# Kernel tuning notes

Measured on AMD Instinct MI355X. Metric: run time of the kernel, lower is better.

Reference implementation:

```python
import jax, jax.numpy as jnp
import numpy as np

B, C_IN, H, W = 4, 256, 64, 64
LATENT = 256


def setup_inputs() -> dict:
    key = jax.random.key(0)
    ks = jax.random.split(key, 12)
    s_in = 1.0 / np.sqrt(C_IN)
    s_lat = 1.0 / np.sqrt(LATENT)
    return {
        "x": jax.random.normal(ks[0], (B, C_IN, H, W), dtype=jnp.float32),
        # 1x1 conv weights stored as [out, in]
        "wq": jax.random.normal(ks[1], (LATENT, C_IN), dtype=jnp.float32) * s_in,
        "bq": jnp.zeros((LATENT,), dtype=jnp.float32),
        "wk": jax.random.normal(ks[2], (LATENT, C_IN), dtype=jnp.float32) * s_in,
        "bk": jnp.zeros((LATENT,), dtype=jnp.float32),
        "wv": jax.random.normal(ks[3], (LATENT, C_IN), dtype=jnp.float32) * s_in,
        "bv": jnp.zeros((LATENT,), dtype=jnp.float32),
        "w_out": jax.random.normal(ks[4], (C_IN, LATENT), dtype=jnp.float32) * s_lat,
        "b_out": jnp.zeros((C_IN,), dtype=jnp.float32),
        # positional-embedding MLP (torch nn.Linear: y = x @ W.T + b)
        "mlp_w1": jax.random.normal(ks[5], (LATENT, LATENT), dtype=jnp.float32) * s_lat,
        "mlp_b1": jnp.zeros((LATENT,), dtype=jnp.float32),
        "mlp_w2": jax.random.normal(ks[6], (LATENT, LATENT), dtype=jnp.float32) * s_lat,
        "mlp_b2": jnp.zeros((LATENT,), dtype=jnp.float32),
    }


def _sinusoidal_table(timesteps, dim):
    # embed[t, d] = sin(arg) if d even else cos(arg), arg = t / 10000**(2d/dim)
    t = jnp.arange(timesteps, dtype=jnp.float32)[:, None]
    p = jnp.arange(dim, dtype=jnp.float32)[None, :]
    w = t / jnp.power(jnp.float32(10000.0), 2.0 * p / dim)
    even = (jnp.arange(dim) % 2 == 0)[None, :]
    return jnp.where(even, jnp.sin(w), jnp.cos(w))  # [T, dim]


def _conv1x1(x, w, b):
    # x: [B, Cin, H, W], w: [Cout, Cin]
    return jnp.einsum('bchw,oc->bohw', x, w) + b[None, :, None, None]


def reference(x, wq, bq, wk, bk, wv, bv, w_out, b_out, mlp_w1, mlp_b1, mlp_w2, mlp_b2):
    batch, _, h, w_ = x.shape
    L = wq.shape[0]
    hw = h * w_

    q = _conv1x1(x, wq, bq)
    k = _conv1x1(x, wk, bk)
    v = _conv1x1(x, wv, bv)

    pe = _sinusoidal_table(hw, L)                     # [HW, L]
    pe = jax.nn.silu(pe @ mlp_w1.T + mlp_b1) @ mlp_w2.T + mlp_b2
    pe = pe.reshape(1, L, h, w_)                      # faithful to torch reshape

    q = (q + pe).reshape(batch, L, hw)
    k = (k + pe).reshape(batch, L, hw)
    v = (v + pe).reshape(batch, L, hw)

    # attention[b, i, j] = sum_c q[b, c, i] * k[b, c, j] / sqrt(L)
    att = jnp.einsum('bci,bcj->bij', q, k) / jnp.sqrt(jnp.float32(L))
    att = jax.nn.softmax(att, axis=1)                 # SAGAN-style: softmax over queries
    res = jnp.einsum('bci,bij->bcj', v, att)          # bmm(v, attention)
    res = res.reshape(batch, L, h, w_)
    return _conv1x1(res, w_out, b_out)
```

## Files before the change

kernel.cpp:

```cpp
#include <hip/hip_runtime.h>
#include <cstdint>


typedef short s8v __attribute__((ext_vector_type(8)));
typedef float f32x4 __attribute__((ext_vector_type(4)));

#define DEVI static __device__ __forceinline__

DEVI unsigned short f2bf(float f) {
  union { float f; uint32_t u; } x; x.f = f;
  uint32_t u = x.u;
  return (unsigned short)((u + 0x7fffu + ((u >> 16) & 1u)) >> 16);
}

DEVI void gl_lds16(const void* g, void* l) {
  __builtin_amdgcn_global_load_lds(
      (const __attribute__((address_space(1))) void*)g,
      (__attribute__((address_space(3))) void*)l,
      16, 0, 0);
}

DEVI void stage(const unsigned short* src, int ld, unsigned short* lds, int t) {
  gl_lds16(src + (long)(t >> 2) * ld + (t & 3) * 8, lds + (t >> 6) * 512);
}

template <int OBF, int BIAS, int PEM, int SILU>
__global__ __launch_bounds__(256) void gemm_nt(
    const unsigned short* __restrict__ A, const unsigned short* __restrict__ B,
    void* __restrict__ Cp, int K, int N, int ld, long sA, long sB, long sC,
    const float* __restrict__ bias, const float* __restrict__ pe, float scale) {
  const int bz = blockIdx.z;
  const unsigned short* Ab = A + (long)bz * sA;
  const unsigned short* Bb = B + (long)bz * sB;
  const int m0 = blockIdx.x * 128, n0 = blockIdx.y * 128;
  __shared__ __align__(16) unsigned short As[4096], Bs[4096];
  const int t = threadIdx.x;
  const int wave = t >> 6, lane = t & 63;
  const int wr = wave >> 1, wc = wave & 1;

  f32x4 acc[4][4];
#pragma unroll
  for (int i = 0; i < 4; i++)
#pragma unroll
    for (int j = 0; j < 4; j++) acc[i][j] = f32x4{0.f, 0.f, 0.f, 0.f};

  const int rl = lane & 15, kp = (lane >> 4) * 8;

  for (int k0 = 0; k0 < K; k0 += 32) {
    stage(Ab + (long)m0 * ld + k0, ld, As, t);
    stage(Ab + (long)(m0 + 64) * ld + k0, ld, As + 2048, t);
    stage(Bb + (long)n0 * ld + k0, ld, Bs, t);
    stage(Bb + (long)(n0 + 64) * ld + k0, ld, Bs + 2048, t);
    __syncthreads();

    s8v af[4], bfr[4];
#pragma unroll
    for (int i = 0; i < 4; i++)
      af[i] = *(const s8v*)(As + (wr * 64 + i * 16 + rl) * 32 + kp);
#pragma unroll
    for (int j = 0; j < 4; j++)
      bfr[j] = *(const s8v*)(Bs + (wc * 64 + j * 16 + rl) * 32 + kp);
#pragma unroll
    for (int i = 0; i < 4; i++)
#pragma unroll
      for (int j = 0; j < 4; j++)
        acc[i][j] = __builtin_amdgcn_mfma_f32_16x16x32_bf16(af[i], bfr[j],
                                                            acc[i][j], 0, 0, 0);
    __syncthreads();
  }

  const long cb = (long)bz * sC;
#pragma unroll
  for (int i = 0; i < 4; i++) {
    const int r0 = m0 + wr * 64 + i * 16 + (lane >> 4) * 4;
#pragma unroll
    for (int j = 0; j < 4; j++) {
      const int col = n0 + wc * 64 + j * 16 + (lane & 15);
#pragma unroll
      for (int r = 0; r < 4; r++) {
        const int row = r0 + r;
        float val = acc[i][j][r] * scale;
        if (BIAS == 1) val += bias[row];
        if (BIAS == 2) val += bias[col];
        if (PEM == 1) val += pe[(long)row * 4096 + col];
        if (PEM == 2) val += pe[(long)col * 4096 + row];
        if (SILU) val = val / (1.0f + __expf(-val));
        const long ci = cb + (long)row * N + col;
        if (OBF)
          ((unsigned short*)Cp)[ci] = f2bf(val);
        else
          ((float*)Cp)[ci] = val;
      }
    }
  }
}

__global__ __launch_bounds__(512, 2) void flash_attn(
    const unsigned short* __restrict__ qTp, const unsigned short* __restrict__ kTp,
    const unsigned short* __restrict__ vBp, float* __restrict__ oPart,
    float* __restrict__ lPart) {
  const int bid = blockIdx.x;
  const int xcd = bid & 7;
  const int b = xcd >> 1, ihalf = xcd & 1;
  const int j0 = (bid >> 3) * 128;
  const long S = 1048576;
  const long ibase = (long)ihalf * 2048;
  const unsigned short* q = qTp + (long)b * S;
  const unsigned short* k = kTp + (long)b * S;
  const unsigned short* v = vBp + (long)b * S;
  const int ob = b * 2 + ihalf;

  __shared__ __align__(16) unsigned char ldsb[151552];

  const int t = threadIdx.x;
  const int wave = t >> 6, lane = t & 63;
  const int jq = wave & 3, ch = wave >> 2;
  const int rl = lane & 15, g = lane >> 4;
  const int kp = g * 8;
  const int ksw = ((g ^ ((rl >> 1) & 3)) << 3);
  const int th = t >> 8, tt = t & 255;
  unsigned short* pL = (unsigned short*)(ldsb + 131072);
  unsigned short* pLw = pL + wave * 1280;

  const unsigned short* krow = k + (long)(j0 + jq * 32 + rl) * 256 + kp;
  s8v kreg[2][8];
#pragma unroll
  for (int jf = 0; jf < 2; jf++)
#pragma unroll
    for (int s = 0; s < 8; s++)
      kreg[jf][s] = *(const s8v*)(krow + jf * 16 * 256 + s * 32);

  f32x4 oacc[2][16];
#pragma unroll
  for (int jf = 0; jf < 2; jf++)
#pragma unroll
    for (int cf = 0; cf < 16; cf++) oacc[jf][cf] = f32x4{0.f, 0.f, 0.f, 0.f};
  float plsum[2][4] = {{0.f, 0.f, 0.f, 0.f}, {0.f, 0.f, 0.f, 0.f}};

  const int tr = tt >> 2, tc = tt & 3;
  const int sc = (tc ^ ((tr >> 1) & 3)) * 8;
  const unsigned short* qsrc[4];
  const unsigned short* vsrc[4];
  const int dsto = (tt >> 6) * 512;
#pragma unroll
  for (int ss = 0; ss < 4; ss++) {
    const int s_ = ss * 2 + th;
    qsrc[ss] = q + ibase * 256 + s_ * 32 + (long)tr * 256 + sc;
    vsrc[ss] = v + (long)((s_ >> 1) * 64) * 4096 + ibase + (s_ & 1) * 32 +
               (long)tr * 4096 + sc;
  }

#define STAGE_QV(bufsel)                                                     \
  {                                                                          \
    unsigned short* qD = (unsigned short*)(ldsb + ((bufsel) << 15));         \
    unsigned short* vD = (unsigned short*)(ldsb + 65536 + ((bufsel) << 15)); \
    _Pragma("unroll") for (int ss = 0; ss < 4; ss++) {                       \
      const int s_ = ss * 2 + th;                                            \
      gl_lds16(qsrc[ss], qD + s_ * 2048 + dsto);                             \
      gl_lds16(vsrc[ss], vD + s_ * 2048 + dsto);                             \
      qsrc[ss] += 16384;                     \
      vsrc[ss] += 64;                        \
    }                                                                        \
  }

  STAGE_QV(0)

  for (int n = 0; n < 32; ++n) {
    const int cur = n & 1;
    __syncthreads();
    if (n + 1 < 32) STAGE_QV(cur ^ 1)

    const unsigned short* qLb = (const unsigned short*)(ldsb + (cur << 15));
    const unsigned short* vLb =
        (const unsigned short*)(ldsb + 65536 + (cur << 15));

    f32x4 sa[2][2];
#pragma unroll
    for (int jf = 0; jf < 2; jf++)
#pragma unroll
      for (int f = 0; f < 2; f++) sa[jf][f] = f32x4{0.f, 0.f, 0.f, 0.f};
    const unsigned short* qbase = qLb + (ch * 32 + rl) * 32 + ksw;
#pragma unroll
    for (int s = 0; s < 8; s++) {
#pragma unroll
      for (int f = 0; f < 2; f++) {
        s8v bf = *(const s8v*)(qbase + s * 2048 + f * 512);
        sa[0][f] = __builtin_amdgcn_mfma_f32_16x16x32_bf16(kreg[0][s], bf,
                                                           sa[0][f], 0, 0, 0);
        sa[1][f] = __builtin_amdgcn_mfma_f32_16x16x32_bf16(kreg[1][s], bf,
                                                           sa[1][f], 0, 0, 0);
      }
    }

#pragma unroll
    for (int jf = 0; jf < 2; jf++)
#pragma unroll
      for (int f = 0; f < 2; f++)
#pragma unroll
        for (int r = 0; r < 4; r++) {
          const float p = __expf(sa[jf][f][r] * 0.0625f);
          plsum[jf][r] += p;
          pLw[jf * 640 + (g * 4 + r) * 40 + f * 16 + rl] = f2bf(p);
        }

    s8v pa0 = *(const s8v*)(pLw + rl * 40 + kp);
    s8v pa1 = *(const s8v*)(pLw + 640 + rl * 40 + kp);
    const unsigned short* vbase = vLb + ch * 2048 + rl * 32 + ksw;
#pragma unroll
    for (int cf = 0; cf < 16; cf++) {
      s8v vb = *(const s8v*)(vbase + (cf >> 2) * 4096 + (cf & 3) * 512);
      oacc[0][cf] = __builtin_amdgcn_mfma_f32_16x16x32_bf16(pa0, vb,
                                                            oacc[0][cf], 0, 0, 0);
      oacc[1][cf] = __builtin_amdgcn_mfma_f32_16x16x32_bf16(pa1, vb,
                                                            oacc[1][cf], 0, 0, 0);
    }
  }

#pragma unroll
  for (int jf = 0; jf < 2; jf++)
#pragma unroll
    for (int r = 0; r < 4; r++) {
      plsum[jf][r] += __shfl_xor(plsum[jf][r], 1);
      plsum[jf][r] += __shfl_xor(plsum[jf][r], 2);
      plsum[jf][r] += __shfl_xor(plsum[jf][r], 4);
      plsum[jf][r] += __shfl_xor(plsum[jf][r], 8);
    }

  __syncthreads();
  float* ex = (float*)ldsb;
  float* exl = (float*)(ldsb + 131072);
  if (ch == 1) {
    float* exw = ex + jq * 8192;
#pragma unroll
    for (int jf = 0; jf < 2; jf++)
#pragma unroll
      for (int cf = 0; cf < 16; cf++)
#pragma unroll
        for (int r = 0; r < 4; r++)
          exw[(jf * 16 + g * 4 + r) * 256 + cf * 16 + rl] = oacc[jf][cf][r];
    if (rl == 0) {
#pragma unroll
      for (int jf = 0; jf < 2; jf++)
#pragma unroll
        for (int r = 0; r < 4; r++)
          exl[jq * 32 + jf * 16 + g * 4 + r] = plsum[jf][r];
    }
  }
  __syncthreads();
  if (ch == 0) {
    float* exw = ex + jq * 8192;
    float* op = oPart + (long)ob * 1048576;
#pragma unroll
    for (int jf = 0; jf < 2; jf++) {
      if (rl == 0) {
#pragma unroll
        for (int r = 0; r < 4; r++) {
          const int jl = jq * 32 + jf * 16 + g * 4 + r;
          lPart[(long)ob * 4096 + j0 + jl] = plsum[jf][r] + exl[jl];
        }
      }
#pragma unroll
      for (int cf = 0; cf < 16; cf++)
#pragma unroll
        for (int r = 0; r < 4; r++) {
          const int jl2 = jf * 16 + g * 4 + r;
          op[(long)(j0 + jq * 32 + jl2) * 256 + cf * 16 + rl] =
              oacc[jf][cf][r] + exw[jl2 * 256 + cf * 16 + rl];
        }
    }
  }
#undef STAGE_QV
}

__global__ __launch_bounds__(256) void combine_o(
    const float* __restrict__ oPart, const float* __restrict__ lPart,
    unsigned short* __restrict__ rT) {
  const long idx = (long)blockIdx.x * 256 + threadIdx.x;
  const int c4 = idx & 63;
  const int j = (idx >> 6) & 4095;
  const int b = idx >> 18;
  const long p0 = ((long)(b * 2) * 1048576 + (long)j * 256) / 4 + c4;
  const float4 a = ((const float4*)oPart)[p0];
  const float4 d = ((const float4*)oPart)[p0 + 262144];
  const float l = lPart[(long)(b * 2) * 4096 + j] +
                  lPart[(long)(b * 2 + 1) * 4096 + j];
  const float inv = 1.0f / l;
  ushort4 o;
  o.x = f2bf((a.x + d.x) * inv);
  o.y = f2bf((a.y + d.y) * inv);
  o.z = f2bf((a.z + d.z) * inv);
  o.w = f2bf((a.w + d.w) * inv);
  ((ushort4*)rT)[(long)b * 262144 + (long)j * 64 + c4] = o;
}

__global__ __launch_bounds__(256) void convert6(
    const float* __restrict__ a0, const float* __restrict__ a1,
    const float* __restrict__ a2, const float* __restrict__ a3,
    const float* __restrict__ a4, const float* __restrict__ a5,
    unsigned short* __restrict__ dst) {
  int idx = blockIdx.x * 256 + threadIdx.x;
  int m = idx >> 16, r = idx & 65535;
  const float* s;
  switch (m) {
    case 0: s = a0; break;
    case 1: s = a1; break;
    case 2: s = a2; break;
    case 3: s = a3; break;
    case 4: s = a4; break;
    default: s = a5; break;
  }
  dst[idx] = f2bf(s[r]);
}

__global__ __launch_bounds__(256) void embed_k(unsigned short* __restrict__ e) {
  int idx = blockIdx.x * 256 + threadIdx.x;
  int t = idx >> 8, d = idx & 255;
  float freq = powf(10000.0f, -(float)d * (1.0f / 128.0f));
  float w = (float)t * freq;
  float r = (d & 1) ? cosf(w) : sinf(w);
  e[idx] = f2bf(r);
}

__global__ void transpose_x(const float* __restrict__ x,
                            unsigned short* __restrict__ xt) {
  __shared__ float tile[32][33];
  const int b = blockIdx.z;
  const int s0 = blockIdx.x * 32, c0 = blockIdx.y * 32;
  const int tx = threadIdx.x, ty = threadIdx.y;
  const float* xb = x + (long)b * 256 * 4096;
#pragma unroll
  for (int r = 0; r < 32; r += 8)
    tile[ty + r][tx] = xb[(long)(c0 + ty + r) * 4096 + s0 + tx];
  __syncthreads();
  unsigned short* xtb = xt + (long)b * 4096 * 256;
#pragma unroll
  for (int r = 0; r < 32; r += 8)
    xtb[(long)(s0 + ty + r) * 256 + c0 + tx] = f2bf(tile[tx][ty + r]);
}

extern "C" void kernel_launch(void* const* d_in, const int* in_sizes, int n_in,
                              void* d_out, int out_size, void* d_ws,
                              size_t ws_size, hipStream_t stream) {
  const float* x  = (const float*)d_in[0];
  const float* wq = (const float*)d_in[1];
  const float* bq = (const float*)d_in[2];
  const float* wk = (const float*)d_in[3];
  const float* bk = (const float*)d_in[4];
  const float* wv = (const float*)d_in[5];
  const float* bv = (const float*)d_in[6];
  const float* wo = (const float*)d_in[7];
  const float* bo = (const float*)d_in[8];
  const float* w1 = (const float*)d_in[9];
  const float* b1 = (const float*)d_in[10];
  const float* w2 = (const float*)d_in[11];
  const float* b2 = (const float*)d_in[12];
  float* out = (float*)d_out;

  char* ws = (char*)d_ws;
  unsigned short* wqb = (unsigned short*)(ws + 0);
  unsigned short* wkb = (unsigned short*)(ws + 131072);
  unsigned short* wvb = (unsigned short*)(ws + 262144);
  unsigned short* wob = (unsigned short*)(ws + 393216);
  unsigned short* w1b = (unsigned short*)(ws + 524288);
  unsigned short* w2b = (unsigned short*)(ws + 655360);
  unsigned short* emb = (unsigned short*)(ws + 786432);
  unsigned short* h1b = (unsigned short*)(ws + 2883584);
  float*          peF = (float*)(ws + 4980736);
  unsigned short* XT  = (unsigned short*)(ws + 9175040);
  unsigned short* qT  = (unsigned short*)(ws + 17563648);
  unsigned short* kT  = (unsigned short*)(ws + 25952256);
  unsigned short* vB  = (unsigned short*)(ws + 34340864);
  unsigned short* rT  = (unsigned short*)(ws + 42729472);
  float*          oP  = (float*)(ws + 51118080);
  float*          lP  = (float*)(ws + 84672512);
  (void)ws_size; (void)in_sizes; (void)n_in; (void)out_size;

  const dim3 B256(256);
  const long S = 1048576;

  convert6<<<1536, B256, 0, stream>>>(wq, wk, wv, wo, w1, w2, wqb);
  embed_k<<<4096, B256, 0, stream>>>(emb);
  gemm_nt<1, 2, 0, 1><<<dim3(32, 2, 1), B256, 0, stream>>>(
      emb, w1b, h1b, 256, 256, 256, 0, 0, 0, b1, nullptr, 1.0f);
  gemm_nt<0, 2, 0, 0><<<dim3(32, 2, 1), B256, 0, stream>>>(
      h1b, w2b, peF, 256, 256, 256, 0, 0, 0, b2, nullptr, 1.0f);
  transpose_x<<<dim3(128, 8, 4), dim3(32, 8), 0, stream>>>(x, XT);
  gemm_nt<1, 2, 2, 0><<<dim3(32, 2, 4), B256, 0, stream>>>(
      XT, wqb, qT, 256, 256, 256, S, 0, S, bq, peF, 1.0f);
  gemm_nt<1, 2, 2, 0><<<dim3(32, 2, 4), B256, 0, stream>>>(
      XT, wkb, kT, 256, 256, 256, S, 0, S, bk, peF, 1.0f);
  gemm_nt<1, 1, 1, 0><<<dim3(2, 32, 4), B256, 0, stream>>>(
      wvb, XT, vB, 256, 4096, 256, 0, S, S, bv, peF, 1.0f);

  flash_attn<<<256, dim3(512), 0, stream>>>(qT, kT, vB, oP, lP);
  combine_o<<<4096, B256, 0, stream>>>(oP, lP, rT);

  gemm_nt<0, 1, 0, 0><<<dim3(2, 32, 4), B256, 0, stream>>>(
      wob, rT, out, 256, 4096, 256, 0, S, S, bo, nullptr, 1.0f);
}
```

Before: 171.4 us.

## Software-pipeline attention loop so PV of previous tile overlaps QK of current

Q and V staging are split so that V for a tile is loaded one iteration later than Q. Each iteration now computes QK MFMAs for tile n, then the PV MFMAs for tile n-1 using probabilities written to LDS in the previous iteration. A final PV step after the loop handles the last tile. This reorders the loop so the exp and LDS write of P no longer sit directly between the two MFMA chains, with the aim of hiding that dependency latency. The exponential is also rewritten as exp2f with the log2(e) factor folded into the scale. One risk: the Q prefetch is no longer guarded on the last iteration, so it reads past the current range and writes into an LDS buffer that is never used.

```diff
diff --git a/kernel.cpp b/kernel.cpp
--- a/kernel.cpp
+++ b/kernel.cpp
@@ -150,36 +150,47 @@
                (long)tr * 4096 + sc;
   }
 
-#define STAGE_QV(bufsel)                                                     \
+#define STAGE_Q(bufsel)                                                      \
   {                                                                          \
     unsigned short* qD = (unsigned short*)(ldsb + ((bufsel) << 15));         \
+    _Pragma("unroll") for (int ss = 0; ss < 4; ss++) {                       \
+      const int s_ = ss * 2 + th;                                            \
+      gl_lds16(qsrc[ss], qD + s_ * 2048 + dsto);                             \
+      qsrc[ss] += 16384;                     \
+    }                                                                        \
+  }
+#define STAGE_V(bufsel)                                                      \
+  {                                                                          \
     unsigned short* vD = (unsigned short*)(ldsb + 65536 + ((bufsel) << 15)); \
     _Pragma("unroll") for (int ss = 0; ss < 4; ss++) {                       \
       const int s_ = ss * 2 + th;                                            \
-      gl_lds16(qsrc[ss], qD + s_ * 2048 + dsto);                             \
       gl_lds16(vsrc[ss], vD + s_ * 2048 + dsto);                             \
-      qsrc[ss] += 16384;                     \
       vsrc[ss] += 64;                        \
     }                                                                        \
   }
 
-  STAGE_QV(0)
+  STAGE_Q(0)
 
   for (int n = 0; n < 32; ++n) {
     const int cur = n & 1;
     __syncthreads();
-    if (n + 1 < 32) STAGE_QV(cur ^ 1)
-
-    const unsigned short* qLb = (const unsigned short*)(ldsb + (cur << 15));
-    const unsigned short* vLb =
-        (const unsigned short*)(ldsb + 65536 + (cur << 15));
+
+    s8v pa0 = {}, pa1 = {};
+    if (n > 0) {
+      pa0 = *(const s8v*)(pLw + rl * 40 + kp);
+      pa1 = *(const s8v*)(pLw + 640 + rl * 40 + kp);
+    }
+
+    STAGE_Q(cur ^ 1)
+    STAGE_V(cur)
 
     f32x4 sa[2][2];
 #pragma unroll
     for (int jf = 0; jf < 2; jf++)
 #pragma unroll
       for (int f = 0; f < 2; f++) sa[jf][f] = f32x4{0.f, 0.f, 0.f, 0.f};
-    const unsigned short* qbase = qLb + (ch * 32 + rl) * 32 + ksw;
+    const unsigned short* qbase =
+        (const unsigned short*)(ldsb + (cur << 15)) + (ch * 32 + rl) * 32 + ksw;
 #pragma unroll
     for (int s = 0; s < 8; s++) {
 #pragma unroll
@@ -192,20 +203,39 @@
       }
     }
 
+    if (n > 0) {
+      const unsigned short* vbase =
+          (const unsigned short*)(ldsb + 65536 + ((cur ^ 1) << 15)) +
+          ch * 2048 + rl * 32 + ksw;
+#pragma unroll
+      for (int cf = 0; cf < 16; cf++) {
+        s8v vb = *(const s8v*)(vbase + (cf >> 2) * 4096 + (cf & 3) * 512);
+        oacc[0][cf] = __builtin_amdgcn_mfma_f32_16x16x32_bf16(
+            pa0, vb, oacc[0][cf], 0, 0, 0);
+        oacc[1][cf] = __builtin_amdgcn_mfma_f32_16x16x32_bf16(
+            pa1, vb, oacc[1][cf], 0, 0, 0);
+      }
+    }
+
 #pragma unroll
     for (int jf = 0; jf < 2; jf++)
 #pragma unroll
       for (int f = 0; f < 2; f++)
 #pragma unroll
         for (int r = 0; r < 4; r++) {
-          const float p = __expf(sa[jf][f][r] * 0.0625f);
+          const float p = exp2f(sa[jf][f][r] * 0.09016844005556021f);
           plsum[jf][r] += p;
           pLw[jf * 640 + (g * 4 + r) * 40 + f * 16 + rl] = f2bf(p);
         }
-
+  }
+
+  __syncthreads();
+  {
     s8v pa0 = *(const s8v*)(pLw + rl * 40 + kp);
     s8v pa1 = *(const s8v*)(pLw + 640 + rl * 40 + kp);
-    const unsigned short* vbase = vLb + ch * 2048 + rl * 32 + ksw;
+    const unsigned short* vbase =
+        (const unsigned short*)(ldsb + 65536 + (1 << 15)) + ch * 2048 +
+        rl * 32 + ksw;
 #pragma unroll
     for (int cf = 0; cf < 16; cf++) {
       s8v vb = *(const s8v*)(vbase + (cf >> 2) * 4096 + (cf & 3) * 512);
@@ -269,7 +299,8 @@
         }
     }
   }
-#undef STAGE_QV
+#undef STAGE_Q
+#undef STAGE_V
 }
 
 __global__ __launch_bounds__(256) void combine_o(
```

Result: no change. 172.9 us (+0.9%).

## Keep softmax probabilities in registers by transposing the score MFMA layout

Applied to the files above, without the earlier changes.

The QK^T MFMA is reordered so each lane's accumulator rows line up with the B-operand layout of a 16x16x16 bf16 MFMA. The exponentiated probabilities are then packed straight into registers for the PV product instead of going through a per-wave LDS scratch buffer. The exponent uses exp2f with log2(e) folded into the scale, and the epilogue exchange and output writes become float4. The last-iteration staging guard is removed, so the final iteration issues an extra prefetch past the data it needs, and the PV step now issues twice as many smaller MFMA instructions.

```diff
diff --git a/kernel.cpp b/kernel.cpp
--- a/kernel.cpp
+++ b/kernel.cpp
@@ -3,6 +3,7 @@
 
 
 typedef short s8v __attribute__((ext_vector_type(8)));
+typedef short s4v __attribute__((ext_vector_type(4)));
 typedef float f32x4 __attribute__((ext_vector_type(4)));
 
 #define DEVI static __device__ __forceinline__
@@ -11,6 +12,18 @@
   union { float f; uint32_t u; } x; x.f = f;
   uint32_t u = x.u;
   return (unsigned short)((u + 0x7fffu + ((u >> 16) & 1u)) >> 16);
+}
+
+DEVI f32x4 mfma16(s4v a, s4v b, f32x4 c) {
+#if __has_builtin(__builtin_amdgcn_mfma_f32_16x16x16_bf16)
+  return __builtin_amdgcn_mfma_f32_16x16x16_bf16(a, b, c, 0, 0, 0);
+#elif __has_builtin(__builtin_amdgcn_mfma_f32_16x16x16bf16_1k)
+  return __builtin_amdgcn_mfma_f32_16x16x16bf16_1k(a, b, c, 0, 0, 0);
+#else
+  asm("s_nop 1\n\tv_mfma_f32_16x16x16_bf16 %0, %1, %2, %0"
+      : "+v"(c) : "v"(a), "v"(b));
+  return c;
+#endif
 }
 
 DEVI void gl_lds16(const void* g, void* l) {
@@ -110,7 +123,7 @@
   const unsigned short* v = vBp + (long)b * S;
   const int ob = b * 2 + ihalf;
 
-  __shared__ __align__(16) unsigned char ldsb[151552];
+  __shared__ __align__(16) unsigned char ldsb[131584];
 
   const int t = threadIdx.x;
   const int wave = t >> 6, lane = t & 63;
@@ -119,8 +132,6 @@
   const int kp = g * 8;
   const int ksw = ((g ^ ((rl >> 1) & 3)) << 3);
   const int th = t >> 8, tt = t & 255;
-  unsigned short* pL = (unsigned short*)(ldsb + 131072);
-  unsigned short* pLw = pL + wave * 1280;
 
   const unsigned short* krow = k + (long)(j0 + jq * 32 + rl) * 256 + kp;
   s8v kreg[2][8];
@@ -130,12 +141,12 @@
     for (int s = 0; s < 8; s++)
       kreg[jf][s] = *(const s8v*)(krow + jf * 16 * 256 + s * 32);
 
-  f32x4 oacc[2][16];
-#pragma unroll
-  for (int jf = 0; jf < 2; jf++)
-#pragma unroll
-    for (int cf = 0; cf < 16; cf++) oacc[jf][cf] = f32x4{0.f, 0.f, 0.f, 0.f};
-  float plsum[2][4] = {{0.f, 0.f, 0.f, 0.f}, {0.f, 0.f, 0.f, 0.f}};
+  f32x4 oacc[16][2];
+#pragma unroll
+  for (int cf = 0; cf < 16; cf++)
+#pragma unroll
+    for (int jf = 0; jf < 2; jf++) oacc[cf][jf] = f32x4{0.f, 0.f, 0.f, 0.f};
+  float plsum[2] = {0.f, 0.f};
 
   const int tr = tt >> 2, tc = tt & 3;
   const int sc = (tc ^ ((tr >> 1) & 3)) * 8;
@@ -168,105 +179,95 @@
   for (int n = 0; n < 32; ++n) {
     const int cur = n & 1;
     __syncthreads();
-    if (n + 1 < 32) STAGE_QV(cur ^ 1)
-
-    const unsigned short* qLb = (const unsigned short*)(ldsb + (cur << 15));
+    STAGE_QV(cur ^ 1)
+
+    f32x4 sa[2][2];
+#pragma unroll
+    for (int f = 0; f < 2; f++)
+#pragma unroll
+      for (int jf = 0; jf < 2; jf++) sa[f][jf] = f32x4{0.f, 0.f, 0.f, 0.f};
+    const unsigned short* qbase =
+        (const unsigned short*)(ldsb + (cur << 15)) + (ch * 32 + rl) * 32 + ksw;
+#pragma unroll
+    for (int s = 0; s < 8; s++) {
+#pragma unroll
+      for (int f = 0; f < 2; f++) {
+        s8v qf = *(const s8v*)(qbase + s * 2048 + f * 512);
+        sa[f][0] = __builtin_amdgcn_mfma_f32_16x16x32_bf16(qf, kreg[0][s],
+                                                           sa[f][0], 0, 0, 0);
+        sa[f][1] = __builtin_amdgcn_mfma_f32_16x16x32_bf16(qf, kreg[1][s],
+                                                           sa[f][1], 0, 0, 0);
+      }
+    }
+
+    s4v pb[2][2];
+#pragma unroll
+    for (int kk = 0; kk < 2; kk++)
+#pragma unroll
+      for (int jf = 0; jf < 2; jf++) {
+        const float p0 = exp2f(sa[kk][jf][0] * 0.09016844005556021f);
+        const float p1 = exp2f(sa[kk][jf][1] * 0.09016844005556021f);
+        const float p2 = exp2f(sa[kk][jf][2] * 0.09016844005556021f);
+        const float p3 = exp2f(sa[kk][jf][3] * 0.09016844005556021f);
+        plsum[jf] += (p0 + p1) + (p2 + p3);
+        s4v pk;
+        pk[0] = (short)f2bf(p0); pk[1] = (short)f2bf(p1);
+        pk[2] = (short)f2bf(p2); pk[3] = (short)f2bf(p3);
+        pb[kk][jf] = pk;
+      }
+
     const unsigned short* vLb =
         (const unsigned short*)(ldsb + 65536 + (cur << 15));
-
-    f32x4 sa[2][2];
-#pragma unroll
-    for (int jf = 0; jf < 2; jf++)
-#pragma unroll
-      for (int f = 0; f < 2; f++) sa[jf][f] = f32x4{0.f, 0.f, 0.f, 0.f};
-    const unsigned short* qbase = qLb + (ch * 32 + rl) * 32 + ksw;
-#pragma unroll
-    for (int s = 0; s < 8; s++) {
-#pragma unroll
-      for (int f = 0; f < 2; f++) {
-        s8v bf = *(const s8v*)(qbase + s * 2048 + f * 512);
-        sa[0][f] = __builtin_amdgcn_mfma_f32_16x16x32_bf16(kreg[0][s], bf,
-                                                           sa[0][f], 0, 0, 0);
-        sa[1][f] = __builtin_amdgcn_mfma_f32_16x16x32_bf16(kreg[1][s], bf,
-                                                           sa[1][f], 0, 0, 0);
+#pragma unroll
+    for (int cf = 0; cf < 16; cf++) {
+      const int vrow = (cf >> 2) * 4096 + ch * 2048 + ((cf & 3) * 16 + rl) * 32;
+#pragma unroll
+      for (int kk = 0; kk < 2; kk++) {
+        const int swz = (((2 * kk + (g >> 1)) ^ ((rl >> 1) & 3)) << 3) +
+                        ((g & 1) << 2);
+        s4v va = *(const s4v*)(vLb + vrow + swz);
+        oacc[cf][0] = mfma16(va, pb[kk][0], oacc[cf][0]);
+        oacc[cf][1] = mfma16(va, pb[kk][1], oacc[cf][1]);
       }
     }
-
-#pragma unroll
-    for (int jf = 0; jf < 2; jf++)
-#pragma unroll
-      for (int f = 0; f < 2; f++)
-#pragma unroll
-        for (int r = 0; r < 4; r++) {
-          const float p = __expf(sa[jf][f][r] * 0.0625f);
-          plsum[jf][r] += p;
-          pLw[jf * 640 + (g * 4 + r) * 40 + f * 16 + rl] = f2bf(p);
-        }
-
-    s8v pa0 = *(const s8v*)(pLw + rl * 40 + kp);
-    s8v pa1 = *(const s8v*)(pLw + 640 + rl * 40 + kp);
-    const unsigned short* vbase = vLb + ch * 2048 + rl * 32 + ksw;
-#pragma unroll
-    for (int cf = 0; cf < 16; cf++) {
-      s8v vb = *(const s8v*)(vbase + (cf >> 2) * 4096 + (cf & 3) * 512);
-      oacc[0][cf] = __builtin_amdgcn_mfma_f32_16x16x32_bf16(pa0, vb,
-                                                            oacc[0][cf], 0, 0, 0);
-      oacc[1][cf] = __builtin_amdgcn_mfma_f32_16x16x32_bf16(pa1, vb,
-                                                            oacc[1][cf], 0, 0, 0);
-    }
-  }
-
-#pragma unroll
-  for (int jf = 0; jf < 2; jf++)
-#pragma unroll
-    for (int r = 0; r < 4; r++) {
-      plsum[jf][r] += __shfl_xor(plsum[jf][r], 1);
-      plsum[jf][r] += __shfl_xor(plsum[jf][r], 2);
-      plsum[jf][r] += __shfl_xor(plsum[jf][r], 4);
-      plsum[jf][r] += __shfl_xor(plsum[jf][r], 8);
-    }
+  }
+  asm volatile("s_nop 7\n\ts_nop 7");
+
+#pragma unroll
+  for (int jf = 0; jf < 2; jf++) {
+    plsum[jf] += __shfl_xor(plsum[jf], 16);
+    plsum[jf] += __shfl_xor(plsum[jf], 32);
+  }
 
   __syncthreads();
-  float* ex = (float*)ldsb;
+  float4* ex = (float4*)ldsb;
   float* exl = (float*)(ldsb + 131072);
   if (ch == 1) {
-    float* exw = ex + jq * 8192;
-#pragma unroll
-    for (int jf = 0; jf < 2; jf++)
+#pragma unroll
+    for (int jf = 0; jf < 2; jf++) {
 #pragma unroll
       for (int cf = 0; cf < 16; cf++)
-#pragma unroll
-        for (int r = 0; r < 4; r++)
-          exw[(jf * 16 + g * 4 + r) * 256 + cf * 16 + rl] = oacc[jf][cf][r];
-    if (rl == 0) {
-#pragma unroll
-      for (int jf = 0; jf < 2; jf++)
-#pragma unroll
-        for (int r = 0; r < 4; r++)
-          exl[jq * 32 + jf * 16 + g * 4 + r] = plsum[jf][r];
+        ex[jq * 2048 + (jf * 16 + rl) * 64 + cf * 4 + g] =
+            float4{oacc[cf][jf][0], oacc[cf][jf][1], oacc[cf][jf][2],
+                   oacc[cf][jf][3]};
+      if (g == 0) exl[jq * 32 + jf * 16 + rl] = plsum[jf];
     }
   }
   __syncthreads();
   if (ch == 0) {
-    float* exw = ex + jq * 8192;
-    float* op = oPart + (long)ob * 1048576;
+    float4* op4 = (float4*)(oPart + (long)ob * 1048576);
 #pragma unroll
     for (int jf = 0; jf < 2; jf++) {
-      if (rl == 0) {
-#pragma unroll
-        for (int r = 0; r < 4; r++) {
-          const int jl = jq * 32 + jf * 16 + g * 4 + r;
-          lPart[(long)ob * 4096 + j0 + jl] = plsum[jf][r] + exl[jl];
-        }
+      const int jl = jq * 32 + jf * 16 + rl;
+      if (g == 0)
+        lPart[(long)ob * 4096 + j0 + jl] = plsum[jf] + exl[jl];
+#pragma unroll
+      for (int cf = 0; cf < 16; cf++) {
+        const float4 o = ex[jq * 2048 + (jf * 16 + rl) * 64 + cf * 4 + g];
+        op4[(long)(j0 + jl) * 64 + cf * 4 + g] =
+            float4{oacc[cf][jf][0] + o.x, oacc[cf][jf][1] + o.y,
+                   oacc[cf][jf][2] + o.z, oacc[cf][jf][3] + o.w};
       }
-#pragma unroll
-      for (int cf = 0; cf < 16; cf++)
-#pragma unroll
-        for (int r = 0; r < 4; r++) {
-          const int jl2 = jf * 16 + g * 4 + r;
-          op[(long)(j0 + jq * 32 + jl2) * 256 + cf * 16 + rl] =
-              oacc[jf][cf][r] + exw[jl2 * 256 + cf * 16 + rl];
-        }
     }
   }
 #undef STAGE_QV
```

Result: slower. 180.8 us (+5.5%).
